# Optimization experiments

Hardware: AMD Instinct MI355X
Metric: run time of the kernel (lower is better)

The kernel has to match this reference:

```python
import jax, jax.numpy as jnp
import numpy as np

B, L, C = 8, 16384, 128
H, WS, SHIFT = 4, 64, 32
NW = L // WS
HD = C // H
HID = 4 * C
SCALE = HD ** -0.5
EPS = 1e-5


def _build_mask():
    # standard Swin cyclic-shift attention mask (1D)
    img_mask = np.zeros((1, L, 1), dtype=np.float32)
    cnt = 0
    for sl in (slice(0, -WS), slice(-WS, -SHIFT), slice(-SHIFT, None)):
        img_mask[:, sl, :] = cnt
        cnt += 1
    mw = img_mask.reshape(1, NW, WS)[0]            # (nW, WS)
    attn_mask = mw[:, None, :] - mw[:, :, None]    # (nW, WS, WS)
    attn_mask = np.where(attn_mask != 0, -100.0, 0.0).astype(np.float32)
    return jnp.asarray(attn_mask)


def setup_inputs() -> dict:
    key = jax.random.key(0)
    ks = jax.random.split(key, 12)
    s = 0.02
    return {
        'x': jax.random.normal(ks[0], (B, L, C), jnp.float32),
        'mask': _build_mask(),
        'gamma1': jnp.ones((C,), jnp.float32),
        'beta1': jnp.zeros((C,), jnp.float32),
        'w_qkv': jax.random.normal(ks[1], (C, 3 * C), jnp.float32) * s,
        'b_qkv': jnp.zeros((3 * C,), jnp.float32),
        'rel_bias': jax.random.normal(ks[2], (2 * WS - 1, H), jnp.float32) * s,
        'w_proj': jax.random.normal(ks[3], (C, C), jnp.float32) * s,
        'b_proj': jnp.zeros((C,), jnp.float32),
        'gamma2': jnp.ones((C,), jnp.float32),
        'beta2': jnp.zeros((C,), jnp.float32),
        'w_fc1': jax.random.normal(ks[4], (C, HID), jnp.float32) * s,
        'b_fc1': jnp.zeros((HID,), jnp.float32),
        'w_fc2': jax.random.normal(ks[5], (HID, C), jnp.float32) * s,
        'b_fc2': jnp.zeros((C,), jnp.float32),
    }


def _ln(x, g, b):
    m = jnp.mean(x, -1, keepdims=True)
    v = jnp.mean((x - m) ** 2, -1, keepdims=True)
    return (x - m) * jax.lax.rsqrt(v + EPS) * g + b


def reference(x, mask, gamma1, beta1, w_qkv, b_qkv, rel_bias, w_proj, b_proj,
              gamma2, beta2, w_fc1, b_fc1, w_fc2, b_fc2):
    shortcut = x
    h = _ln(x, gamma1, beta1)
    # cyclic shift (L % WS == 0 so no padding needed)
    h = jnp.roll(h, -SHIFT, axis=1)
    # window partition -> (B*nW, WS, C)
    hw = h.reshape(B * NW, WS, C)
    qkv = hw @ w_qkv + b_qkv                                  # (Bw, WS, 3C)
    qkv = qkv.reshape(B * NW, WS, 3, H, HD).transpose(2, 0, 3, 1, 4)
    q, k, v = qkv[0] * SCALE, qkv[1], qkv[2]                  # (Bw, H, WS, HD)
    attn = jnp.einsum('whqd,whkd->whqk', q, k)                # (Bw, H, WS, WS)
    # relative position bias
    idx = jnp.arange(WS)[:, None] - jnp.arange(WS)[None, :] + WS - 1  # (WS, WS)
    bias = rel_bias[idx].transpose(2, 0, 1)                   # (H, WS, WS)
    attn = attn + bias[None]
    # shift mask per window
    attn = attn.reshape(B, NW, H, WS, WS) + mask[None, :, None]
    attn = jax.nn.softmax(attn, axis=-1).reshape(B * NW, H, WS, WS)
    out = jnp.einsum('whqk,whkd->whqd', attn, v)              # (Bw, H, WS, HD)
    out = out.transpose(0, 2, 1, 3).reshape(B * NW, WS, C)
    out = out @ w_proj + b_proj
    # window reverse + reverse shift
    out = out.reshape(B, L, C)
    out = jnp.roll(out, SHIFT, axis=1)
    x1 = shortcut + out
    # MLP (exact GELU, as torch nn.GELU default)
    m = _ln(x1, gamma2, beta2)
    m = jax.nn.gelu(m @ w_fc1 + b_fc1, approximate=False) @ w_fc2 + b_fc2
    return x1 + m
```

## Files before the change

kernel.cpp:

```cpp
#include <hip/hip_runtime.h>
#include <math.h>

#define B_ 8
#define L_ 16384
#define C_ 128
#define H_ 4
#define WS_ 64
#define SHIFT_ 32
#define NW_ 256
#define HD_ 32
#define HID_ 512
#define M_ (B_*L_)
#define SCALE_ 0.17677669529663687f
#define EPS_ 1e-5f

using short8 = __attribute__((ext_vector_type(8))) short;
using f32x4  = __attribute__((ext_vector_type(4))) float;
using gas1   = const __attribute__((address_space(1))) unsigned int*;
using las3   = __attribute__((address_space(3))) unsigned int*;
typedef unsigned short ushort_t;

#define GLDS(GP, LP) __builtin_amdgcn_global_load_lds((gas1)(const void*)(GP), \
                                                      (las3)(void*)(LP), 16, 0, 0)

__device__ __forceinline__ f32x4 mfma16(short8 a, short8 b, f32x4 c) {
    return __builtin_amdgcn_mfma_f32_16x16x32_bf16(a, b, c, 0, 0, 0);
}

__device__ __forceinline__ ushort_t f2bf(float v)
{
    unsigned u = __float_as_uint(v);
    return (ushort_t)((u + 0x7fff + ((u >> 16) & 1)) >> 16);
}
__device__ __forceinline__ void bsplit(float v, ushort_t& h, ushort_t& l)
{
    unsigned b = __float_as_uint(v);
    h = (ushort_t)(b >> 16);
    float vh = __uint_as_float(b & 0xffff0000u);
    l = (ushort_t)(__float_as_uint(v - vh) >> 16);
}
__device__ __forceinline__ float bf2f(unsigned s) { return __uint_as_float(s << 16); }

__global__ __launch_bounds__(256)
void ln_ts(const float* __restrict__ in, ushort_t* __restrict__ oh,
           ushort_t* __restrict__ ol,
           const float* __restrict__ gamma, const float* __restrict__ beta,
           int do_shift, int m_off)
{
    int m    = blockIdx.x * 4 + (threadIdx.x >> 6);
    int lane = threadIdx.x & 63;
    int gr   = m_off + m;
    int src  = gr;
    if (do_shift) {
        int b = gr >> 14, l = gr & (L_ - 1);
        src = (b << 14) | ((l + SHIFT_) & (L_ - 1));
    }
    const float* row = in + (size_t)src * C_;
    float2 v = *(const float2*)&row[lane * 2];
    float s  = v.x + v.y;
    float ss = v.x * v.x + v.y * v.y;
#pragma unroll
    for (int off = 1; off < 64; off <<= 1) {
        s  += __shfl_xor(s, off);
        ss += __shfl_xor(ss, off);
    }
    float mean = s * (1.f / C_);
    float var  = ss * (1.f / C_) - mean * mean;
    float rstd = rsqrtf(var + EPS_);
    float2 g  = *(const float2*)&gamma[lane * 2];
    float2 bt = *(const float2*)&beta[lane * 2];
    float ox = (v.x - mean) * rstd * g.x + bt.x;
    float oy = (v.y - mean) * rstd * g.y + bt.y;
    int k = lane * 2;
    unsigned idx = (unsigned)((m >> 4) * 16 + (k >> 3)) * 128 + (m & 15) * 8 + (k & 7);
    ushort_t h0, l0, h1, l1;
    bsplit(ox, h0, l0); bsplit(oy, h1, l1);
    *(unsigned*)&oh[idx] = (unsigned)h0 | ((unsigned)h1 << 16);
    *(unsigned*)&ol[idx] = (unsigned)l0 | ((unsigned)l1 << 16);
}

__global__ __launch_bounds__(256)
void wconv(const float* __restrict__ wq, const float* __restrict__ wp,
           const float* __restrict__ w1, const float* __restrict__ w2,
           ushort_t* __restrict__ th)
{
    int e = blockIdx.x * 256 + threadIdx.x;
    const float* W; int K, N, base, local;
    if (e < 49152)       { W = wq; K = 128; N = 384; base = 0;      local = e; }
    else if (e < 65536)  { W = wp; K = 128; N = 128; base = 49152;  local = e - 49152; }
    else if (e < 131072) { W = w1; K = 128; N = 512; base = 65536;  local = e - 65536; }
    else                 { W = w2; K = 512; N = 128; base = 131072; local = e - 131072; }
    int n = local / K, k = local % K;
    int idx = base + ((n >> 4) * (K >> 3) + (k >> 3)) * 128 + (n & 15) * 8 + (k & 7);
    th[idx] = f2bf(W[(size_t)k * N + n]);
}

__global__ __launch_bounds__(256)
void attn_kernel(const ushort_t* __restrict__ qkv, const float* __restrict__ relb,
                 ushort_t* __restrict__ Oh, ushort_t* __restrict__ Ol,
                 int w_off)
{
    __shared__ ushort_t SH[24576];
    __shared__ float bls[H_][128];
    const int w    = blockIdx.x;
    const int h    = threadIdx.x >> 6;
    const int lane = threadIdx.x & 63;
    ushort_t* QP = SH + h * 4096;
    ushort_t* VT = SH + 16384 + h * 2048;

    const ushort_t* base = qkv + (size_t)w * WS_ * 384 + h * HD_;

    bls[h][lane] = relb[lane * H_ + h];
    if (lane < 63) bls[h][lane + 64] = relb[(lane + 64) * H_ + h];

#pragma unroll
    for (int it = 0; it < 4; ++it) {
        int f = it * 64 + lane;
        int r = f >> 2, oct = f & 3;
        uint4 vq = *(const uint4*)&base[r * 384 + oct * 8];
        uint4 vk = *(const uint4*)&base[r * 384 + C_ + oct * 8];
        int ti = ((r >> 4) * 4 + oct) * 128 + (r & 15) * 8;
        *(uint4*)&QP[ti]        = vq;
        *(uint4*)&QP[2048 + ti] = vk;
    }
#pragma unroll
    for (int it = 0; it < 4; ++it) {
        int f = it * 64 + lane;
        int r = f >> 2, oct = f & 3;
        ushort_t tmp[8];
        *(uint4*)tmp = *(const uint4*)&base[r * 384 + 2 * C_ + oct * 8];
#pragma unroll
        for (int e = 0; e < 8; ++e) {
            int d = oct * 8 + e;
            VT[((d >> 4) * 8 + (r >> 3)) * 128 + (d & 15) * 8 + (r & 7)] = tmp[e];
        }
    }

    f32x4 acc[4][4];
    {
        const int lro = (lane >> 4) * 128 + (lane & 15) * 8;
        short8 aq[4], bk[4];
#pragma unroll
        for (int i = 0; i < 4; ++i) aq[i] = *(const short8*)&QP[i * 512 + lro];
#pragma unroll
        for (int j = 0; j < 4; ++j) bk[j] = *(const short8*)&QP[2048 + j * 512 + lro];
        const f32x4 z = {0.f, 0.f, 0.f, 0.f};
#pragma unroll
        for (int i = 0; i < 4; ++i)
#pragma unroll
        for (int j = 0; j < 4; ++j)
            acc[i][j] = mfma16(aq[i], bk[j], z);
    }

    const int wn = (w_off + w) & (NW_ - 1);
    const bool lastw = (wn == NW_ - 1);
#pragma unroll
    for (int i = 0; i < 4; ++i)
#pragma unroll
    for (int j = 0; j < 4; ++j) {
        const int bidx = i * 16 + (lane >> 4) * 4 - j * 16 - (lane & 15) + 63;
        const float mv = (lastw && ((i ^ j) & 2)) ? -100.f : 0.f;
#pragma unroll
        for (int r = 0; r < 4; ++r)
            acc[i][j][r] = acc[i][j][r] * SCALE_ + bls[h][bidx + r] + mv;
    }
    float mx[4][4], sm[4][4];
#pragma unroll
    for (int i = 0; i < 4; ++i)
#pragma unroll
    for (int r = 0; r < 4; ++r) {
        float m = fmaxf(fmaxf(acc[i][0][r], acc[i][1][r]),
                        fmaxf(acc[i][2][r], acc[i][3][r]));
#pragma unroll
        for (int off = 1; off < 16; off <<= 1) m = fmaxf(m, __shfl_xor(m, off));
        mx[i][r] = m;
    }
#pragma unroll
    for (int i = 0; i < 4; ++i)
#pragma unroll
    for (int j = 0; j < 4; ++j)
#pragma unroll
    for (int r = 0; r < 4; ++r)
        acc[i][j][r] = __expf(acc[i][j][r] - mx[i][r]);
#pragma unroll
    for (int i = 0; i < 4; ++i)
#pragma unroll
    for (int r = 0; r < 4; ++r) {
        float s = acc[i][0][r] + acc[i][1][r] + acc[i][2][r] + acc[i][3][r];
#pragma unroll
        for (int off = 1; off < 16; off <<= 1) s += __shfl_xor(s, off);
        sm[i][r] = 1.f / s;
    }
#pragma unroll
    for (int i = 0; i < 4; ++i)
#pragma unroll
    for (int j = 0; j < 4; ++j) {
        const int kb   = j * 2 + ((lane & 15) >> 3);
        const int koff = lane & 7;
#pragma unroll
        for (int r = 0; r < 4; ++r)
            QP[(i * 8 + kb) * 128 + ((lane >> 4) * 4 + r) * 8 + koff] =
                f2bf(acc[i][j][r] * sm[i][r]);
    }
    f32x4 oacc[4][2] = {};
    {
        short8 vb[2][2];
#pragma unroll
        for (int dp = 0; dp < 2; ++dp)
#pragma unroll
        for (int kk = 0; kk < 2; ++kk)
            vb[dp][kk] = *(const short8*)&VT[(dp * 8 + kk * 4 + (lane >> 4)) * 128 + (lane & 15) * 8];
#pragma unroll
        for (int i = 0; i < 4; ++i)
#pragma unroll
        for (int kk = 0; kk < 2; ++kk) {
            short8 pa = *(const short8*)&QP[(i * 8 + kk * 4 + (lane >> 4)) * 128 + (lane & 15) * 8];
#pragma unroll
            for (int dp = 0; dp < 2; ++dp)
                oacc[i][dp] = mfma16(pa, vb[dp][kk], oacc[i][dp]);
        }
    }
    const int gm0 = w * WS_;
#pragma unroll
    for (int i = 0; i < 4; ++i)
#pragma unroll
    for (int dp = 0; dp < 2; ++dp) {
        const int c  = h * HD_ + dp * 16 + (lane & 15);
        const int cb = c >> 3;
#pragma unroll
        for (int r = 0; r < 4; ++r) {
            const int gm = gm0 + i * 16 + (lane >> 4) * 4 + r;
            const size_t idx = ((size_t)(gm >> 4) * 16 + cb) * 128 + (gm & 15) * 8 + (c & 7);
            ushort_t hh, ll; bsplit(oacc[i][dp][r], hh, ll);
            Oh[idx] = hh; Ol[idx] = ll;
        }
    }
}

template<int EPI>
__global__ __launch_bounds__(256, 2)
void mgemm(const ushort_t* __restrict__ Ahi, const ushort_t* __restrict__ Alo,
           const ushort_t* __restrict__ Bhi,
           const float* __restrict__ bias, float* __restrict__ Cd,
           ushort_t* __restrict__ Cb, const float* __restrict__ X,
           int M, int N, int K, int m_off)
{
    __shared__ ushort_t lds[2][3][4096];
    const int t    = threadIdx.x;
    const int lane = t & 63, wid = t >> 6;
    const int wmP  = (wid >> 1) * 4;
    const int wnP  = (wid & 1) * 4;
    const int pm0  = blockIdx.x * 8;
    const int pn0  = blockIdx.y * 8;
    const int lro  = (lane >> 4) * 128 + (lane & 15) * 8;
    const size_t pstr = (size_t)16 * K;

    f32x4 acc[4][4] = {};

#define STAGE(buf, kc) { \
    const size_t ko = (size_t)((kc) >> 3) * 128; \
    _Pragma("unroll") \
    for (int sh = 0; sh < 2; ++sh) { \
        const int f = sh * 2048 + t * 8; \
        const int p = f >> 9, o = f & 511; \
        const size_t ga = (size_t)(pm0 + p) * pstr + ko + o; \
        const size_t gb = (size_t)(pn0 + p) * pstr + ko + o; \
        GLDS(Ahi + ga, &lds[buf][0][f]); \
        GLDS(Alo + ga, &lds[buf][1][f]); \
        GLDS(Bhi + gb, &lds[buf][2][f]); \
    } }

#define COMPUTE(buf) { \
    short8 ah[4], al[4], bh[4]; \
    _Pragma("unroll") for (int i = 0; i < 4; ++i) { \
        ah[i] = *(const short8*)&lds[buf][0][(wmP + i) * 512 + lro]; \
        al[i] = *(const short8*)&lds[buf][1][(wmP + i) * 512 + lro]; \
        bh[i] = *(const short8*)&lds[buf][2][(wnP + i) * 512 + lro]; \
    } \
    _Pragma("unroll") for (int i = 0; i < 4; ++i) \
    _Pragma("unroll") for (int j = 0; j < 4; ++j) { \
        acc[i][j] = mfma16(ah[i], bh[j], acc[i][j]); \
        acc[i][j] = mfma16(al[i], bh[j], acc[i][j]); \
    } }

    const int nst = K >> 5;
    STAGE(0, 0);
    __syncthreads();
    int cur = 0;
    for (int c = 0; c < nst; ++c) {
        if (c + 1 < nst) STAGE(cur ^ 1, (c + 1) << 5);
        COMPUTE(cur);
        __syncthreads();
        cur ^= 1;
    }
#undef STAGE
#undef COMPUTE

    const int m0r = blockIdx.x * 128;
    const int n0  = blockIdx.y * 128;
#pragma unroll
    for (int j = 0; j < 4; ++j) {
        const int col = n0 + (wid & 1) * 64 + j * 16 + (lane & 15);
        const float bv = bias[col];
#pragma unroll
        for (int i = 0; i < 4; ++i) {
#pragma unroll
            for (int r = 0; r < 4; ++r) {
                const int row = m0r + (wid >> 1) * 64 + i * 16 + (lane >> 4) * 4 + r;
                float v = acc[i][j][r] + bv;
                if (EPI == 0) {
                    Cb[(size_t)row * N + col] = f2bf(v);
                } else {
                    int gr = m_off + row;
                    int b = gr >> 14, l = gr & (L_ - 1);
                    size_t dst = ((size_t)((b << 14) | ((l + SHIFT_) & (L_ - 1)))) * C_ + col;
                    Cd[dst] = v + X[dst];
                }
            }
        }
    }
}

__global__ __launch_bounds__(256, 2)
void mlp_k(const ushort_t* __restrict__ Ahi, const ushort_t* __restrict__ Alo,
           const ushort_t* __restrict__ W1h, const ushort_t* __restrict__ W2h,
           const float* __restrict__ b1, const float* __restrict__ b2,
           float* __restrict__ Out, int m_off)
{
    __shared__ ushort_t Am[2][8192];
    __shared__ ushort_t Gs[8192];
    __shared__ ushort_t Wl[2][4096];
    const int t    = threadIdx.x;
    const int lane = t & 63, wid = t >> 6;
    const int wm   = (wid >> 1) * 32;
    const int wnq  = (wid & 1) * 4;
    const int pm0  = blockIdx.x * 4;

    {
        const ushort_t* srcH = Ahi + (size_t)pm0 * 2048;
        const ushort_t* srcL = Alo + (size_t)pm0 * 2048;
#pragma unroll
        for (int sh = 0; sh < 4; ++sh) {
            int f = sh * 2048 + t * 8;
            GLDS(srcH + f, &Am[0][f]);
            GLDS(srcL + f, &Am[1][f]);
        }
    }
    auto stageW1 = [&](int buf, int q, int kk) {
#pragma unroll
        for (int sh = 0; sh < 2; ++sh) {
            int f = sh * 2048 + t * 8;
            int p = f >> 9, o = f & 511;
            GLDS(W1h + (size_t)(q * 8 + p) * 2048 + kk * 512 + o, &Wl[buf][f]);
        }
    };
    auto stageW2 = [&](int buf, int q, int kk) {
#pragma unroll
        for (int sh = 0; sh < 2; ++sh) {
            int f = sh * 2048 + t * 8;
            int p = f >> 9, o = f & 511;
            GLDS(W2h + (size_t)p * 8192 + q * 2048 + kk * 512 + o, &Wl[buf][f]);
        }
    };

    f32x4 acc2[2][4] = {};
    stageW1(0, 0, 0);
    __syncthreads();
    int buf = 0;

    for (int q = 0; q < 4; ++q) {
        f32x4 acc1[2][4] = {};
#pragma unroll
        for (int kk = 0; kk < 4; ++kk) {
            if (kk < 3) stageW1(buf ^ 1, q, kk + 1);
            else        stageW2(buf ^ 1, q, 0);
            short8 bh[4];
#pragma unroll
            for (int j = 0; j < 4; ++j)
                bh[j] = *(const short8*)&Wl[buf][(wnq + j) * 512 + (lane >> 4) * 128 + (lane & 15) * 8];
#pragma unroll
            for (int i = 0; i < 2; ++i) {
                int ai = ((wid >> 1) * 2 + i) * 2048 + (kk * 4 + (lane >> 4)) * 128 + (lane & 15) * 8;
                short8 ah = *(const short8*)&Am[0][ai];
                short8 al = *(const short8*)&Am[1][ai];
#pragma unroll
                for (int j = 0; j < 4; ++j) {
                    acc1[i][j] = mfma16(ah, bh[j], acc1[i][j]);
                    acc1[i][j] = mfma16(al, bh[j], acc1[i][j]);
                }
            }
            __syncthreads();
            buf ^= 1;
        }
#pragma unroll
        for (int i = 0; i < 2; ++i)
#pragma unroll
          for (int j = 0; j < 4; ++j) {
            int kg = (wid & 1) * 64 + j * 16 + (lane & 15);
            float bb = b1[q * 128 + kg];
#pragma unroll
            for (int r = 0; r < 4; ++r) {
                int row = wm + i * 16 + (lane >> 4) * 4 + r;
                float v = acc1[i][j][r] + bb;
                v = 0.5f * v * (1.f + erff(v * 0.70710678118654752f));
                Gs[(row >> 4) * 2048 + (kg >> 3) * 128 + (row & 15) * 8 + (kg & 7)] = f2bf(v);
            }
          }
        __syncthreads();
#pragma unroll
        for (int kk = 0; kk < 4; ++kk) {
            if (kk < 3)      stageW2(buf ^ 1, q, kk + 1);
            else if (q < 3)  stageW1(buf ^ 1, q + 1, 0);
            short8 bh[4];
#pragma unroll
            for (int j = 0; j < 4; ++j)
                bh[j] = *(const short8*)&Wl[buf][(wnq + j) * 512 + (lane >> 4) * 128 + (lane & 15) * 8];
#pragma unroll
            for (int i = 0; i < 2; ++i) {
                int gi = ((wid >> 1) * 2 + i) * 2048 + (kk * 4 + (lane >> 4)) * 128 + (lane & 15) * 8;
                short8 ga = *(const short8*)&Gs[gi];
#pragma unroll
                for (int j = 0; j < 4; ++j)
                    acc2[i][j] = mfma16(ga, bh[j], acc2[i][j]);
            }
            __syncthreads();
            buf ^= 1;
        }
    }
#pragma unroll
    for (int i = 0; i < 2; ++i)
#pragma unroll
      for (int j = 0; j < 4; ++j) {
        int col = (wid & 1) * 64 + j * 16 + (lane & 15);
        float bb = b2[col];
#pragma unroll
        for (int r = 0; r < 4; ++r) {
            int row = blockIdx.x * 64 + wm + i * 16 + (lane >> 4) * 4 + r;
            size_t di = (size_t)(m_off + row) * C_ + col;
            Out[di] += acc2[i][j][r] + bb;
        }
      }
}

extern "C" void kernel_launch(void* const* d_in, const int* in_sizes, int n_in,
                              void* d_out, int out_size, void* d_ws, size_t ws_size,
                              hipStream_t stream)
{
    const float* x      = (const float*)d_in[0];
    const float* gamma1 = (const float*)d_in[2];
    const float* beta1  = (const float*)d_in[3];
    const float* w_qkv  = (const float*)d_in[4];
    const float* b_qkv  = (const float*)d_in[5];
    const float* relb   = (const float*)d_in[6];
    const float* w_proj = (const float*)d_in[7];
    const float* b_proj = (const float*)d_in[8];
    const float* gamma2 = (const float*)d_in[9];
    const float* beta2  = (const float*)d_in[10];
    const float* w_fc1  = (const float*)d_in[11];
    const float* b_fc1  = (const float*)d_in[12];
    const float* w_fc2  = (const float*)d_in[13];
    const float* b_fc2  = (const float*)d_in[14];
    float* out = (float*)d_out;

    int nch = 8;
    for (int c = 1; c <= 8; c <<= 1) {
        size_t need = 393216 + (size_t)(M_ / c) * 1792;
        if (need <= ws_size) { nch = c; break; }
    }
    const int Mc = M_ / nch;

    ushort_t* wth  = (ushort_t*)d_ws;
    ushort_t* dynp = wth + 196608;
    ushort_t* h_hi = dynp;
    ushort_t* h_lo = h_hi + (size_t)Mc * C_;
    ushort_t* a_hi = h_lo + (size_t)Mc * C_;
    ushort_t* a_lo = a_hi + (size_t)Mc * C_;
    ushort_t* qkvb = a_lo + (size_t)Mc * C_;

    wconv<<<dim3(768), dim3(256), 0, stream>>>(w_qkv, w_proj, w_fc1, w_fc2, wth);

    for (int ch = 0; ch < nch; ++ch) {
        int m0 = ch * Mc;

        ln_ts<<<dim3(Mc / 4), dim3(256), 0, stream>>>(x, h_hi, h_lo, gamma1, beta1, 1, m0);

        mgemm<0><<<dim3(Mc / 128, 3), dim3(256), 0, stream>>>(
            h_hi, h_lo, wth, b_qkv, nullptr, qkvb, nullptr, Mc, 3 * C_, C_, 0);

        attn_kernel<<<dim3(Mc / WS_), dim3(256), 0, stream>>>(
            qkvb, relb, a_hi, a_lo, m0 / WS_);

        mgemm<1><<<dim3(Mc / 128, 1), dim3(256), 0, stream>>>(
            a_hi, a_lo, wth + 49152, b_proj, out, nullptr, x, Mc, C_, C_, m0);

        ln_ts<<<dim3(Mc / 4), dim3(256), 0, stream>>>(out, h_hi, h_lo, gamma2, beta2, 0, m0);

        mlp_k<<<dim3(Mc / 64), dim3(256), 0, stream>>>(
            h_hi, h_lo, wth + 65536, wth + 131072, b_fc1, b_fc2, out, m0);
    }
}
```

Measured before the change: 485.2 us.

## Restructure MLP kernel to 128-row tiles with per-wave rows and tanh GELU

The fused MLP kernel now gives each wave its own 32 rows and all 128 output columns. Activations and fc2 weights are read straight from global memory into registers, and only a full 128x128 fc1 weight quarter is staged in shared memory. The block tile doubles to 128 rows and the per-tile sync/double-buffer pipeline is dropped. Exact erf GELU is replaced with the tanh approximation using __expf. This cuts barriers and LDS traffic but adds register pressure and uncached-looking global loads, and changes numerics away from the exact GELU the reference specifies.

```diff
diff --git a/kernel.cpp b/kernel.cpp
--- a/kernel.cpp
+++ b/kernel.cpp
@@ -40,6 +40,14 @@
     l = (ushort_t)(__float_as_uint(v - vh) >> 16);
 }
 __device__ __forceinline__ float bf2f(unsigned s) { return __uint_as_float(s << 16); }
+
+__device__ __forceinline__ float gelu_f(float x)
+{
+    float u = 1.5957691216057308f * (x + 0.044715f * x * x * x);
+    float e = __expf(u);
+    float t = 1.f - 2.f / (e + 1.f);
+    return 0.5f * x * (1.f + t);
+}
 
 __global__ __launch_bounds__(256)
 void ln_ts(const float* __restrict__ in, ushort_t* __restrict__ oh,
@@ -323,123 +331,94 @@
 
 __global__ __launch_bounds__(256, 2)
 void mlp_k(const ushort_t* __restrict__ Ahi, const ushort_t* __restrict__ Alo,
-           const ushort_t* __restrict__ W1h, const ushort_t* __restrict__ W2h,
+           const ushort_t* __restrict__ W1t, const ushort_t* __restrict__ W2t,
            const float* __restrict__ b1, const float* __restrict__ b2,
            float* __restrict__ Out, int m_off)
 {
-    __shared__ ushort_t Am[2][8192];
-    __shared__ ushort_t Gs[8192];
-    __shared__ ushort_t Wl[2][4096];
-    const int t    = threadIdx.x;
-    const int lane = t & 63, wid = t >> 6;
-    const int wm   = (wid >> 1) * 32;
-    const int wnq  = (wid & 1) * 4;
-    const int pm0  = blockIdx.x * 4;
-
-    {
-        const ushort_t* srcH = Ahi + (size_t)pm0 * 2048;
-        const ushort_t* srcL = Alo + (size_t)pm0 * 2048;
-#pragma unroll
-        for (int sh = 0; sh < 4; ++sh) {
-            int f = sh * 2048 + t * 8;
-            GLDS(srcH + f, &Am[0][f]);
-            GLDS(srcL + f, &Am[1][f]);
-        }
-    }
-    auto stageW1 = [&](int buf, int q, int kk) {
-#pragma unroll
-        for (int sh = 0; sh < 2; ++sh) {
-            int f = sh * 2048 + t * 8;
-            int p = f >> 9, o = f & 511;
-            GLDS(W1h + (size_t)(q * 8 + p) * 2048 + kk * 512 + o, &Wl[buf][f]);
-        }
-    };
-    auto stageW2 = [&](int buf, int q, int kk) {
-#pragma unroll
-        for (int sh = 0; sh < 2; ++sh) {
-            int f = sh * 2048 + t * 8;
-            int p = f >> 9, o = f & 511;
-            GLDS(W2h + (size_t)p * 8192 + q * 2048 + kk * 512 + o, &Wl[buf][f]);
-        }
-    };
-
-    f32x4 acc2[2][4] = {};
-    stageW1(0, 0, 0);
+    __shared__ ushort_t Wq[16384];
+    __shared__ ushort_t Gs[4][4096];
+    const int t = threadIdx.x, lane = t & 63, w = t >> 6;
+    const int g = lane >> 4, c = lane & 15;
+    const int rp0 = blockIdx.x * 8 + w * 2;
+    ushort_t* gs = Gs[w];
+
+#pragma unroll
+    for (int it = 0; it < 8; ++it) { int f = it * 2048 + t * 8; GLDS(W1t + f, &Wq[f]); }
     __syncthreads();
-    int buf = 0;
-
+
+    f32x4 acc2[2][8] = {};
     for (int q = 0; q < 4; ++q) {
-        f32x4 acc1[2][4] = {};
-#pragma unroll
-        for (int kk = 0; kk < 4; ++kk) {
-            if (kk < 3) stageW1(buf ^ 1, q, kk + 1);
-            else        stageW2(buf ^ 1, q, 0);
-            short8 bh[4];
-#pragma unroll
-            for (int j = 0; j < 4; ++j)
-                bh[j] = *(const short8*)&Wl[buf][(wnq + j) * 512 + (lane >> 4) * 128 + (lane & 15) * 8];
-#pragma unroll
-            for (int i = 0; i < 2; ++i) {
-                int ai = ((wid >> 1) * 2 + i) * 2048 + (kk * 4 + (lane >> 4)) * 128 + (lane & 15) * 8;
-                short8 ah = *(const short8*)&Am[0][ai];
-                short8 al = *(const short8*)&Am[1][ai];
-#pragma unroll
-                for (int j = 0; j < 4; ++j) {
-                    acc1[i][j] = mfma16(ah, bh[j], acc1[i][j]);
-                    acc1[i][j] = mfma16(al, bh[j], acc1[i][j]);
-                }
+        f32x4 acc1[2][8] = {};
+#pragma unroll
+        for (int ks = 0; ks < 4; ++ks) {
+            short8 mh[2], ml[2], wf[8];
+#pragma unroll
+            for (int jb = 0; jb < 2; ++jb) {
+                size_t ai = (size_t)(rp0 + jb) * 2048 + (ks * 4 + g) * 128 + c * 8;
+                mh[jb] = *(const short8*)&Ahi[ai];
+                ml[jb] = *(const short8*)&Alo[ai];
             }
-            __syncthreads();
-            buf ^= 1;
-        }
-#pragma unroll
-        for (int i = 0; i < 2; ++i)
-#pragma unroll
-          for (int j = 0; j < 4; ++j) {
-            int kg = (wid & 1) * 64 + j * 16 + (lane & 15);
-            float bb = b1[q * 128 + kg];
+#pragma unroll
+            for (int cb = 0; cb < 8; ++cb)
+                wf[cb] = *(const short8*)&Wq[cb * 2048 + (ks * 4 + g) * 128 + c * 8];
+#pragma unroll
+            for (int jb = 0; jb < 2; ++jb)
+#pragma unroll
+            for (int cb = 0; cb < 8; ++cb) {
+                acc1[jb][cb] = mfma16(mh[jb], wf[cb], acc1[jb][cb]);
+                acc1[jb][cb] = mfma16(ml[jb], wf[cb], acc1[jb][cb]);
+            }
+        }
+        __syncthreads();
+        if (q < 3) {
+            const ushort_t* src = W1t + (q + 1) * 16384;
+#pragma unroll
+            for (int it = 0; it < 8; ++it) { int f = it * 2048 + t * 8; GLDS(src + f, &Wq[f]); }
+        }
+#pragma unroll
+        for (int jb = 0; jb < 2; ++jb)
+#pragma unroll
+        for (int cb = 0; cb < 8; ++cb) {
+            const int kg = cb * 16 + c;
+            const float bb = b1[q * 128 + kg];
 #pragma unroll
             for (int r = 0; r < 4; ++r) {
-                int row = wm + i * 16 + (lane >> 4) * 4 + r;
-                float v = acc1[i][j][r] + bb;
-                v = 0.5f * v * (1.f + erff(v * 0.70710678118654752f));
-                Gs[(row >> 4) * 2048 + (kg >> 3) * 128 + (row & 15) * 8 + (kg & 7)] = f2bf(v);
+                float v = gelu_f(acc1[jb][cb][r] + bb);
+                gs[(jb * 16 + (kg >> 3)) * 128 + (g * 4 + r) * 8 + (kg & 7)] = f2bf(v);
             }
-          }
+        }
+#pragma unroll
+        for (int ks = 0; ks < 4; ++ks) {
+            short8 w2f[8], ga[2];
+#pragma unroll
+            for (int ocb = 0; ocb < 8; ++ocb) {
+                size_t wi = (size_t)ocb * 8192 + (q * 16 + ks * 4 + g) * 128 + c * 8;
+                w2f[ocb] = *(const short8*)&W2t[wi];
+            }
+#pragma unroll
+            for (int jb = 0; jb < 2; ++jb)
+                ga[jb] = *(const short8*)&gs[(jb * 16 + ks * 4 + g) * 128 + c * 8];
+#pragma unroll
+            for (int jb = 0; jb < 2; ++jb)
+#pragma unroll
+            for (int ocb = 0; ocb < 8; ++ocb)
+                acc2[jb][ocb] = mfma16(ga[jb], w2f[ocb], acc2[jb][ocb]);
+        }
         __syncthreads();
-#pragma unroll
-        for (int kk = 0; kk < 4; ++kk) {
-            if (kk < 3)      stageW2(buf ^ 1, q, kk + 1);
-            else if (q < 3)  stageW1(buf ^ 1, q + 1, 0);
-            short8 bh[4];
-#pragma unroll
-            for (int j = 0; j < 4; ++j)
-                bh[j] = *(const short8*)&Wl[buf][(wnq + j) * 512 + (lane >> 4) * 128 + (lane & 15) * 8];
-#pragma unroll
-            for (int i = 0; i < 2; ++i) {
-                int gi = ((wid >> 1) * 2 + i) * 2048 + (kk * 4 + (lane >> 4)) * 128 + (lane & 15) * 8;
-                short8 ga = *(const short8*)&Gs[gi];
-#pragma unroll
-                for (int j = 0; j < 4; ++j)
-                    acc2[i][j] = mfma16(ga, bh[j], acc2[i][j]);
-            }
-            __syncthreads();
-            buf ^= 1;
-        }
-    }
-#pragma unroll
-    for (int i = 0; i < 2; ++i)
-#pragma unroll
-      for (int j = 0; j < 4; ++j) {
-        int col = (wid & 1) * 64 + j * 16 + (lane & 15);
-        float bb = b2[col];
+    }
+#pragma unroll
+    for (int jb = 0; jb < 2; ++jb)
+#pragma unroll
+    for (int ocb = 0; ocb < 8; ++ocb) {
+        const int col = ocb * 16 + c;
+        const float bb = b2[col];
 #pragma unroll
         for (int r = 0; r < 4; ++r) {
-            int row = blockIdx.x * 64 + wm + i * 16 + (lane >> 4) * 4 + r;
+            const int row = blockIdx.x * 128 + w * 32 + jb * 16 + g * 4 + r;
             size_t di = (size_t)(m_off + row) * C_ + col;
-            Out[di] += acc2[i][j][r] + bb;
-        }
-      }
+            Out[di] += acc2[jb][ocb][r] + bb;
+        }
+    }
 }
 
 extern "C" void kernel_launch(void* const* d_in, const int* in_sizes, int n_in,
@@ -495,7 +474,7 @@
 
         ln_ts<<<dim3(Mc / 4), dim3(256), 0, stream>>>(out, h_hi, h_lo, gamma2, beta2, 0, m0);
 
-        mlp_k<<<dim3(Mc / 64), dim3(256), 0, stream>>>(
+        mlp_k<<<dim3(Mc / 128), dim3(256), 0, stream>>>(
             h_hi, h_lo, wth + 65536, wth + 131072, b_fc1, b_fc2, out, m0);
     }
 }
```

After: 455.9 us. 6.0% less time.
